# Performance work log

Measured on AMD Instinct MI355X. Metric: run time of the kernel, lower is better.

The kernel has to match this reference:

```python
import jax, jax.numpy as jnp
import numpy as np

MASK_VALUE = 0.0  # default `mask=0` scalar in the original forward


def setup_inputs() -> dict:
    key = jax.random.key(0)
    kq, kk, kv = jax.random.split(key, 3)
    b, n, d_k, d_v = 8, 2048, 64, 64
    q = jax.random.normal(kq, (b, n, d_k), dtype=jnp.float32)
    k = jax.random.normal(kk, (b, n, d_k), dtype=jnp.float32)
    v = jax.random.normal(kv, (b, n, d_v), dtype=jnp.float32)
    return {"q": q, "k": k, "v": v}


def reference(q, k, v):
    d_k = q.shape[-1]
    temper = jnp.asarray(d_k, q.dtype) ** 0.5
    # scores: (b, n, n)
    attn = jnp.einsum('bqd,bkd->bqk', q, k) / temper
    # equality-based masking: positions whose score exactly equals the
    # scalar `mask` (default 0) are set to -inf before softmax.
    attn = jnp.where(attn == MASK_VALUE, -jnp.inf, attn)
    # NOTE: the original code calls `attn.masked_fill(look_ahead_mask==0, -inf)`
    # WITHOUT assignment, so the look-ahead mask is a no-op; we omit it faithfully.
    attn = jax.nn.softmax(attn, axis=-1)
    out = jnp.einsum('bqk,bkd->bqd', attn, v)  # (b, n, d_v)
    return out
```

## Files before the change

kernel.cpp:

```cpp
#include <hip/hip_runtime.h>
#include <hip/hip_bf16.h>

typedef __bf16 bf16_t;
typedef bf16_t bf16x8 __attribute__((ext_vector_type(8)));
typedef bf16_t bf16x4 __attribute__((ext_vector_type(4)));
typedef float  floatx4  __attribute__((ext_vector_type(4)));
typedef float  floatx16 __attribute__((ext_vector_type(16)));

constexpr int B = 8, N = 2048, D = 64;
constexpr int KSTR = 72;
constexpr int VSTR = 136;
constexpr int PSTR = 40;
constexpr int OSTR = 68;
constexpr int TSTR = 65;

__global__ __launch_bounds__(256)
void prepass_kernel(const float* __restrict__ k, const float* __restrict__ v,
                    bf16_t* __restrict__ kb, bf16_t* __restrict__ vt) {
    __shared__ float t[64 * TSTR];
    const int tid = threadIdx.x;
    const int r0  = blockIdx.x * 64;
    const int b   = blockIdx.y;
    if (blockIdx.z == 0) {
        const float* src = k + ((size_t)b * N + r0) * D;
        bf16_t* dst = kb + ((size_t)b * N + r0) * D;
        #pragma unroll
        for (int p = 0; p < 4; ++p) {
            int e = (tid + p * 256) * 4;
            floatx4 f = *(const floatx4*)(src + e);
            bf16x4 o;
            #pragma unroll
            for (int j = 0; j < 4; ++j) o[j] = (bf16_t)f[j];
            *(bf16x4*)(dst + e) = o;
        }
    } else {
        const float* vb = v + ((size_t)b * N + r0) * D;
        #pragma unroll
        for (int p = 0; p < 4; ++p) {
            int e = (tid + p * 256) * 4;
            int row = e >> 6, col = e & 63;
            floatx4 f = *(const floatx4*)(vb + e);
            #pragma unroll
            for (int j = 0; j < 4; ++j) t[(col + j) * TSTR + row] = f[j];
        }
        __syncthreads();
        bf16_t* ob = vt + (size_t)b * D * N + r0;
        #pragma unroll
        for (int p = 0; p < 4; ++p) {
            int e = (tid + p * 256) * 4;
            int drow = e >> 6, kcol = e & 63;
            bf16x4 o;
            #pragma unroll
            for (int j = 0; j < 4; ++j) o[j] = (bf16_t)t[drow * TSTR + kcol + j];
            *(bf16x4*)(ob + (size_t)drow * N + kcol) = o;
        }
    }
}

__global__ __launch_bounds__(256, 3)
void attn_kernel(const float* __restrict__ q, const bf16_t* __restrict__ kb,
                 const bf16_t* __restrict__ vt, float* __restrict__ out) {
    __shared__ char smem[18432 + 17408 + 10240];
    bf16_t* lds_k = (bf16_t*)smem;
    bf16_t* lds_v = (bf16_t*)(smem + 18432);
    bf16_t* lds_p = (bf16_t*)(smem + 18432 + 17408);
    float*  o_buf = (float*)smem;
    float*  l_buf = (float*)(smem + 26112);

    const int tid = threadIdx.x;
    const int lane = tid & 63;
    const int cg  = tid >> 6;
    const int h   = lane >> 5;
    const int l31 = lane & 31;

    const int b  = blockIdx.y;
    const int q0 = blockIdx.x * 32;

    const bf16_t* kbb = kb + (size_t)b * N * D;
    const bf16_t* vbb = vt + (size_t)b * D * N;

    bf16x8 qf[4];
    {
        const float* qp = q + ((size_t)b * N + q0 + l31) * D + h * 8;
        #pragma unroll
        for (int kd = 0; kd < 4; ++kd) {
            floatx4 f0 = *(const floatx4*)(qp + kd * 16);
            floatx4 f1 = *(const floatx4*)(qp + kd * 16 + 4);
            bf16x8 t;
            #pragma unroll
            for (int j = 0; j < 4; ++j) { t[j] = (bf16_t)f0[j]; t[j + 4] = (bf16_t)f1[j]; }
            qf[kd] = t;
        }
    }

    floatx16 o_acc[2];
    #pragma unroll
    for (int d = 0; d < 2; ++d)
        #pragma unroll
        for (int i = 0; i < 16; ++i) o_acc[d][i] = 0.f;
    float l_run[16];
    #pragma unroll
    for (int i = 0; i < 16; ++i) l_run[i] = 0.f;

    bf16x8 kreg[4], vreg[4];
    #pragma unroll
    for (int p = 0; p < 4; ++p) {
        kreg[p] = *(const bf16x8*)(kbb + (size_t)(tid + p * 256) * 8);
        int e = (tid + p * 256) * 8;
        vreg[p] = *(const bf16x8*)(vbb + (size_t)(e >> 7) * N + (e & 127));
    }

    bf16_t* pw = lds_p + cg * 32 * PSTR;

    #pragma unroll 1
    for (int it = 0; it < N / 128; ++it) {
        __syncthreads();
        #pragma unroll
        for (int p = 0; p < 4; ++p) {
            int e = (tid + p * 256) * 8;
            *(bf16x8*)&lds_k[(e >> 6) * KSTR + (e & 63)] = kreg[p];
            *(bf16x8*)&lds_v[(e >> 7) * VSTR + (e & 127)] = vreg[p];
        }
        __syncthreads();
        if (it + 1 < N / 128) {
            const int kv1 = (it + 1) * 128;
            #pragma unroll
            for (int p = 0; p < 4; ++p) {
                int e = (tid + p * 256) * 8;
                kreg[p] = *(const bf16x8*)(kbb + (size_t)kv1 * D + e);
                vreg[p] = *(const bf16x8*)(vbb + (size_t)(e >> 7) * N + kv1 + (e & 127));
            }
        }

        floatx16 s;
        #pragma unroll
        for (int i = 0; i < 16; ++i) s[i] = 0.f;
        #pragma unroll
        for (int kd = 0; kd < 4; ++kd) {
            bf16x8 kf = *(const bf16x8*)&lds_k[(cg * 32 + l31) * KSTR + kd * 16 + h * 8];
            s = __builtin_amdgcn_mfma_f32_32x32x16_bf16(qf[kd], kf, s, 0, 0, 0);
        }

        #pragma unroll
        for (int i = 0; i < 16; ++i) {
            const int row = (i & 3) + 8 * (i >> 2) + 4 * h;
            float x = s[i] * 0.125f;
            float p = (x == 0.0f) ? 0.0f : __expf(x);
            l_run[i] += p;
            pw[row * PSTR + l31] = (bf16_t)p;
        }

        #pragma unroll
        for (int s2 = 0; s2 < 2; ++s2) {
            bf16x8 pa = *(const bf16x8*)&pw[l31 * PSTR + s2 * 16 + h * 8];
            #pragma unroll
            for (int dsub = 0; dsub < 2; ++dsub) {
                bf16x8 vf = *(const bf16x8*)&lds_v[(dsub * 32 + l31) * VSTR + cg * 32 + s2 * 16 + h * 8];
                o_acc[dsub] = __builtin_amdgcn_mfma_f32_32x32x16_bf16(pa, vf, o_acc[dsub], 0, 0, 0);
            }
        }
    }

    __syncthreads();

    #pragma unroll
    for (int i = 0; i < 16; ++i) {
        float x = l_run[i];
        x += __shfl_xor(x, 1);
        x += __shfl_xor(x, 2);
        x += __shfl_xor(x, 4);
        x += __shfl_xor(x, 8);
        x += __shfl_xor(x, 16);
        l_run[i] = x;
    }

    if (cg > 0) {
        float* ob = o_buf + (size_t)(cg - 1) * 32 * OSTR;
        #pragma unroll
        for (int dsub = 0; dsub < 2; ++dsub)
            #pragma unroll
            for (int i = 0; i < 16; ++i) {
                const int row = (i & 3) + 8 * (i >> 2) + 4 * h;
                ob[row * OSTR + dsub * 32 + l31] = o_acc[dsub][i];
            }
        if (l31 == 0)
            #pragma unroll
            for (int i = 0; i < 16; ++i) {
                const int row = (i & 3) + 8 * (i >> 2) + 4 * h;
                l_buf[(cg - 1) * 32 + row] = l_run[i];
            }
    }
    __syncthreads();
    if (cg == 0) {
        float* op = out + ((size_t)b * N + q0) * D;
        #pragma unroll
        for (int i = 0; i < 16; ++i) {
            const int row = (i & 3) + 8 * (i >> 2) + 4 * h;
            const float inv_l = 1.0f / (l_run[i] + l_buf[row] + l_buf[32 + row] + l_buf[64 + row]);
            #pragma unroll
            for (int dsub = 0; dsub < 2; ++dsub) {
                float sum = o_acc[dsub][i];
                #pragma unroll
                for (int g = 0; g < 3; ++g)
                    sum += o_buf[(size_t)g * 32 * OSTR + row * OSTR + dsub * 32 + l31];
                op[(size_t)row * D + dsub * 32 + l31] = sum * inv_l;
            }
        }
    }
}

extern "C" void kernel_launch(void* const* d_in, const int* in_sizes, int n_in,
                              void* d_out, int out_size, void* d_ws, size_t ws_size,
                              hipStream_t stream) {
    const float* q = (const float*)d_in[0];
    const float* k = (const float*)d_in[1];
    const float* v = (const float*)d_in[2];
    float* out = (float*)d_out;
    bf16_t* kb = (bf16_t*)d_ws;
    bf16_t* vt = (bf16_t*)((char*)d_ws + (size_t)B * N * D * 2);

    hipLaunchKernelGGL(prepass_kernel, dim3(N / 64, B, 2), dim3(256), 0, stream, k, v, kb, vt);
    hipLaunchKernelGGL(attn_kernel, dim3(N / 32, B), dim3(256), 0, stream, q, kb, vt, out);
}
```

Measured before the change: 93.66 us.

## Compute transposed S so P stays in registers, dropping LDS round-trip

The QK^T MFMA now swaps its operands to produce S^T, so each lane holds the scores for a single query row. The exponentiated P values are packed to bf16 in registers and exchanged across wave halves with shuffles to form the B operand of the PV MFMA, replacing the LDS write and read of P. This cuts LDS traffic and shared memory use, lets the row sum become a single scalar per lane, and allows occupancy to rise from 3 to 4 blocks. The epilogue is rewritten for the transposed output layout and uses vectorized float4 stores. The cost is extra cross-lane shuffles and selects in every iteration, plus added register pressure under the tighter launch bound.

```diff
diff --git a/kernel.cpp b/kernel.cpp
--- a/kernel.cpp
+++ b/kernel.cpp
@@ -2,16 +2,15 @@
 #include <hip/hip_bf16.h>
 
 typedef __bf16 bf16_t;
+typedef bf16_t bf16x2 __attribute__((ext_vector_type(2)));
+typedef bf16_t bf16x4 __attribute__((ext_vector_type(4)));
 typedef bf16_t bf16x8 __attribute__((ext_vector_type(8)));
-typedef bf16_t bf16x4 __attribute__((ext_vector_type(4)));
 typedef float  floatx4  __attribute__((ext_vector_type(4)));
 typedef float  floatx16 __attribute__((ext_vector_type(16)));
 
 constexpr int B = 8, N = 2048, D = 64;
 constexpr int KSTR = 72;
 constexpr int VSTR = 136;
-constexpr int PSTR = 40;
-constexpr int OSTR = 68;
 constexpr int TSTR = 65;
 
 __global__ __launch_bounds__(256)
@@ -57,21 +56,19 @@
     }
 }
 
-__global__ __launch_bounds__(256, 3)
+__global__ __launch_bounds__(256, 4)
 void attn_kernel(const float* __restrict__ q, const bf16_t* __restrict__ kb,
                  const bf16_t* __restrict__ vt, float* __restrict__ out) {
-    __shared__ char smem[18432 + 17408 + 10240];
-    bf16_t* lds_k = (bf16_t*)smem;
-    bf16_t* lds_v = (bf16_t*)(smem + 18432);
-    bf16_t* lds_p = (bf16_t*)(smem + 18432 + 17408);
-    float*  o_buf = (float*)smem;
-    float*  l_buf = (float*)(smem + 26112);
-
-    const int tid = threadIdx.x;
+    __shared__ bf16_t lds_k[128 * KSTR];
+    __shared__ bf16_t lds_v[64 * VSTR];
+    __shared__ float  l_buf[3][32];
+    float* o_buf = (float*)lds_k;
+
+    const int tid  = threadIdx.x;
     const int lane = tid & 63;
-    const int cg  = tid >> 6;
-    const int h   = lane >> 5;
-    const int l31 = lane & 31;
+    const int cg   = tid >> 6;
+    const int h    = lane >> 5;
+    const int l31  = lane & 31;
 
     const int b  = blockIdx.y;
     const int q0 = blockIdx.x * 32;
@@ -98,19 +95,15 @@
     for (int d = 0; d < 2; ++d)
         #pragma unroll
         for (int i = 0; i < 16; ++i) o_acc[d][i] = 0.f;
-    float l_run[16];
-    #pragma unroll
-    for (int i = 0; i < 16; ++i) l_run[i] = 0.f;
+    float l_run = 0.f;
 
     bf16x8 kreg[4], vreg[4];
     #pragma unroll
     for (int p = 0; p < 4; ++p) {
-        kreg[p] = *(const bf16x8*)(kbb + (size_t)(tid + p * 256) * 8);
         int e = (tid + p * 256) * 8;
+        kreg[p] = *(const bf16x8*)(kbb + e);
         vreg[p] = *(const bf16x8*)(vbb + (size_t)(e >> 7) * N + (e & 127));
     }
-
-    bf16_t* pw = lds_p + cg * 32 * PSTR;
 
     #pragma unroll 1
     for (int it = 0; it < N / 128; ++it) {
@@ -138,74 +131,77 @@
         #pragma unroll
         for (int kd = 0; kd < 4; ++kd) {
             bf16x8 kf = *(const bf16x8*)&lds_k[(cg * 32 + l31) * KSTR + kd * 16 + h * 8];
-            s = __builtin_amdgcn_mfma_f32_32x32x16_bf16(qf[kd], kf, s, 0, 0, 0);
-        }
-
-        #pragma unroll
-        for (int i = 0; i < 16; ++i) {
-            const int row = (i & 3) + 8 * (i >> 2) + 4 * h;
-            float x = s[i] * 0.125f;
-            float p = (x == 0.0f) ? 0.0f : __expf(x);
-            l_run[i] += p;
-            pw[row * PSTR + l31] = (bf16_t)p;
+            s = __builtin_amdgcn_mfma_f32_32x32x16_bf16(kf, qf[kd], s, 0, 0, 0);
+        }
+
+        int q8[8];
+        #pragma unroll
+        for (int g = 0; g < 8; ++g) {
+            union { int i; bf16x2 h2; } u;
+            #pragma unroll
+            for (int j = 0; j < 2; ++j) {
+                float x = s[2 * g + j] * 0.125f;
+                float p = (x == 0.0f) ? 0.0f : __expf(x);
+                l_run += p;
+                u.h2[j] = (bf16_t)p;
+            }
+            q8[g] = u.i;
         }
 
         #pragma unroll
         for (int s2 = 0; s2 < 2; ++s2) {
-            bf16x8 pa = *(const bf16x8*)&pw[l31 * PSTR + s2 * 16 + h * 8];
-            #pragma unroll
-            for (int dsub = 0; dsub < 2; ++dsub) {
-                bf16x8 vf = *(const bf16x8*)&lds_v[(dsub * 32 + l31) * VSTR + cg * 32 + s2 * 16 + h * 8];
-                o_acc[dsub] = __builtin_amdgcn_mfma_f32_32x32x16_bf16(pa, vf, o_acc[dsub], 0, 0, 0);
+            int r0 = __shfl_xor(q8[4 * s2 + 0], 32);
+            int r1 = __shfl_xor(q8[4 * s2 + 1], 32);
+            int r2 = __shfl_xor(q8[4 * s2 + 2], 32);
+            int r3 = __shfl_xor(q8[4 * s2 + 3], 32);
+            union { int i4[4]; bf16x8 v; } bf;
+            bf.i4[0] = h ? r2 : q8[4 * s2 + 0];
+            bf.i4[1] = h ? r3 : q8[4 * s2 + 1];
+            bf.i4[2] = h ? q8[4 * s2 + 2] : r0;
+            bf.i4[3] = h ? q8[4 * s2 + 3] : r1;
+            #pragma unroll
+            for (int dblk = 0; dblk < 2; ++dblk) {
+                bf16x8 va = *(const bf16x8*)&lds_v[(dblk * 32 + l31) * VSTR + cg * 32 + s2 * 16 + h * 8];
+                o_acc[dblk] = __builtin_amdgcn_mfma_f32_32x32x16_bf16(va, bf.v, o_acc[dblk], 0, 0, 0);
             }
         }
     }
 
     __syncthreads();
 
-    #pragma unroll
-    for (int i = 0; i < 16; ++i) {
-        float x = l_run[i];
-        x += __shfl_xor(x, 1);
-        x += __shfl_xor(x, 2);
-        x += __shfl_xor(x, 4);
-        x += __shfl_xor(x, 8);
-        x += __shfl_xor(x, 16);
-        l_run[i] = x;
-    }
+    l_run += __shfl_xor(l_run, 32);
 
     if (cg > 0) {
-        float* ob = o_buf + (size_t)(cg - 1) * 32 * OSTR;
-        #pragma unroll
-        for (int dsub = 0; dsub < 2; ++dsub)
+        float* ob = o_buf + (size_t)(cg - 1) * 64 * 32;
+        #pragma unroll
+        for (int dblk = 0; dblk < 2; ++dblk)
             #pragma unroll
             for (int i = 0; i < 16; ++i) {
-                const int row = (i & 3) + 8 * (i >> 2) + 4 * h;
-                ob[row * OSTR + dsub * 32 + l31] = o_acc[dsub][i];
-            }
-        if (l31 == 0)
-            #pragma unroll
-            for (int i = 0; i < 16; ++i) {
-                const int row = (i & 3) + 8 * (i >> 2) + 4 * h;
-                l_buf[(cg - 1) * 32 + row] = l_run[i];
-            }
+                const int d = (i & 3) + 8 * (i >> 2) + 4 * h + dblk * 32;
+                ob[d * 32 + l31] = o_acc[dblk][i];
+            }
+        if (h == 0) l_buf[cg - 1][l31] = l_run;
     }
     __syncthreads();
     if (cg == 0) {
-        float* op = out + ((size_t)b * N + q0) * D;
-        #pragma unroll
-        for (int i = 0; i < 16; ++i) {
-            const int row = (i & 3) + 8 * (i >> 2) + 4 * h;
-            const float inv_l = 1.0f / (l_run[i] + l_buf[row] + l_buf[32 + row] + l_buf[64 + row]);
-            #pragma unroll
-            for (int dsub = 0; dsub < 2; ++dsub) {
-                float sum = o_acc[dsub][i];
+        const float inv_l = 1.0f / (l_run + l_buf[0][l31] + l_buf[1][l31] + l_buf[2][l31]);
+        float* op = out + ((size_t)b * N + q0 + l31) * D;
+        #pragma unroll
+        for (int dblk = 0; dblk < 2; ++dblk)
+            #pragma unroll
+            for (int g = 0; g < 4; ++g) {
+                const int d0 = 8 * g + 4 * h + dblk * 32;
+                floatx4 o4;
                 #pragma unroll
-                for (int g = 0; g < 3; ++g)
-                    sum += o_buf[(size_t)g * 32 * OSTR + row * OSTR + dsub * 32 + l31];
-                op[(size_t)row * D + dsub * 32 + l31] = sum * inv_l;
-            }
-        }
+                for (int j = 0; j < 4; ++j) {
+                    float sum = o_acc[dblk][4 * g + j];
+                    #pragma unroll
+                    for (int gg = 0; gg < 3; ++gg)
+                        sum += o_buf[(size_t)gg * 64 * 32 + (d0 + j) * 32 + l31];
+                    o4[j] = sum * inv_l;
+                }
+                *(floatx4*)(op + d0) = o4;
+            }
     }
 }
 
```

Measured after the change: 91.22 us. -2.6%, faster.
